# Optimization experiments

Hardware: AMD Instinct MI355X
Metric: run time of the kernel (lower is better)

## Reference

```python
import jax, jax.numpy as jnp
import numpy as np
from jax.scipy.linalg import cho_solve

B, IN, H, Y, K = 16384, 128, 512, 32, 8
EPS = 1e-6


def setup_inputs() -> dict:
    key = jax.random.key(0)
    ks = jax.random.split(key, 7)
    s_in = 1.0 / np.sqrt(IN)
    s_h = 1.0 / np.sqrt(H)
    x = jax.random.normal(ks[0], (B, IN), dtype=jnp.float32)
    W1 = jax.random.normal(ks[1], (IN, H), dtype=jnp.float32) * s_in
    b1 = jnp.zeros((H,), dtype=jnp.float32)
    WD = jax.random.normal(ks[2], (H, Y), dtype=jnp.float32) * s_h
    bD = jnp.zeros((Y,), dtype=jnp.float32)
    WV = jax.random.normal(ks[3], (H, Y * K), dtype=jnp.float32) * s_h
    bV = jnp.zeros((Y * K,), dtype=jnp.float32)
    return {"x": x, "W1": W1, "b1": b1, "WD": WD, "bD": bD, "WV": WV, "bV": bV}


def reference(x, W1, b1, WD, bD, WV, bV):
    # backbone: simple MLP feature extractor
    feat = jax.nn.relu(x @ W1 + b1)                      # [B, H]
    # head (low_rank mode): D > 0 diagonal scales, V low-rank factor
    D = jax.nn.softplus(feat @ WD + bD) + 1e-3           # [B, Y]
    V = (feat @ WV + bV).reshape(-1, Y, K)               # [B, Y, K]

    inv_D2 = 1.0 / (D * D)                               # [B, Y]
    W = V * inv_D2[..., None]                            # A_inv @ V, [B, Y, K]
    # M = I_K + V^T A_inv V  (Woodbury capacitance), [B, K, K]
    M = jnp.eye(K, dtype=V.dtype) + jnp.einsum("byk,byj->bkj", V, W)
    L_M = jnp.linalg.cholesky(M)
    eyeK = jnp.broadcast_to(jnp.eye(K, dtype=V.dtype), M.shape)
    M_inv = cho_solve((L_M, True), eyeK)                 # torch.cholesky_inverse
    # Sigma_inv = A_inv - W M_inv W^T, [B, Y, Y]
    correction = jnp.einsum("byk,bkj,bzj->byz", W, M_inv, W)
    A_inv = inv_D2[:, :, None] * jnp.eye(Y, dtype=V.dtype)
    Sigma_inv = A_inv - correction

    eigvals, eigvecs = jnp.linalg.eigh(Sigma_inv)        # [B,Y], [B,Y,Y]
    sqrt_vals = jnp.sqrt(eigvals + EPS)
    # Sigma_inv_sqrt = Q diag(sqrt(lam)) Q^T
    Sigma_inv_sqrt = jnp.einsum("byk,bk,bzk->byz", eigvecs, sqrt_vals, eigvecs)
    return Sigma_inv_sqrt
```

## Files before the change

kernel.cpp:

```cpp
#include <hip/hip_runtime.h>
#include <math.h>


template <int ACT>
__global__ __launch_bounds__(256) void gemm_act(const float* __restrict__ A,
                                                const float* __restrict__ Bm,
                                                const float* __restrict__ bias,
                                                float* __restrict__ C,
                                                int M, int N, int K) {
  __shared__ float As[16][68];
  __shared__ float Bs[16][68];
  const int tid = threadIdx.x;
  const int bm = blockIdx.y * 64;
  const int bn = blockIdx.x * 64;
  const int tx = tid & 15, ty = tid >> 4;
  const int arow = tid >> 2, acol4 = (tid & 3) << 2;
  const int brow = tid >> 4, bcol4 = (tid & 15) << 2;
  float acc[4][4] = {};

  for (int k0 = 0; k0 < K; k0 += 16) {
    float4 av = *(const float4*)(A + (size_t)(bm + arow) * K + (k0 + acol4));
    As[acol4 + 0][arow] = av.x;
    As[acol4 + 1][arow] = av.y;
    As[acol4 + 2][arow] = av.z;
    As[acol4 + 3][arow] = av.w;
    float4 bv = make_float4(0.f, 0.f, 0.f, 0.f);
    if (bn + bcol4 < N)
      bv = *(const float4*)(Bm + (size_t)(k0 + brow) * N + (bn + bcol4));
    *(float4*)&Bs[brow][bcol4] = bv;
    __syncthreads();
#pragma unroll
    for (int k = 0; k < 16; ++k) {
      float ar[4], br[4];
#pragma unroll
      for (int i = 0; i < 4; ++i) ar[i] = As[k][(ty << 2) + i];
#pragma unroll
      for (int j = 0; j < 4; ++j) br[j] = Bs[k][(tx << 2) + j];
#pragma unroll
      for (int i = 0; i < 4; ++i)
#pragma unroll
        for (int j = 0; j < 4; ++j) acc[i][j] = fmaf(ar[i], br[j], acc[i][j]);
    }
    __syncthreads();
  }

#pragma unroll
  for (int i = 0; i < 4; ++i) {
    int row = bm + (ty << 2) + i;
#pragma unroll
    for (int j = 0; j < 4; ++j) {
      int col = bn + (tx << 2) + j;
      if (col < N) {
        float v = acc[i][j] + bias[col];
        if (ACT == 1) v = fmaxf(v, 0.f);
        if (ACT == 2) {
          float sp = fmaxf(v, 0.f) + log1pf(expf(-fabsf(v)));
          float D = sp + 1e-3f;
          v = 1.f / (D * D);
        }
        C[(size_t)row * N + col] = v;
      }
    }
  }
}

__global__ __launch_bounds__(64) void woodbury_sqrtm_os(
    const float* __restrict__ invD2g, const float* __restrict__ Vg,
    float* __restrict__ out) {
  const int lane = threadIdx.x;
  const int h = lane >> 5;
  const int j = lane & 31;
  const int b = blockIdx.x * 2 + h;

  __shared__ __align__(16) char lds[9216];
  float* Vb = (float*)lds;
  float* ad = (float*)(lds + 2048);
  double* Md = (double*)(lds + 2304);
  double* Ud = (double*)(lds + 3456);
  float* FT = (float*)lds;

  const float a_d = invD2g[(size_t)b * 32 + j];
  const float4 v0 = *(const float4*)(Vg + (size_t)b * 256 + j * 8);
  const float4 v1 = *(const float4*)(Vg + (size_t)b * 256 + j * 8 + 4);
  {
    float* vb = Vb + (h * 32 + j) * 8;
    *(float4*)vb = v0;
    *(float4*)(vb + 4) = v1;
    ad[h * 32 + j] = a_d;
  }
  __syncthreads();

  {
    const int e0 = 2 * j;
    const int i0 = e0 >> 3, c0 = e0 & 7;
    double m0 = (i0 == c0) ? 1.0 : 0.0;
    double m1 = (i0 == c0 + 1) ? 1.0 : 0.0;
    const float* vbase = Vb + h * 256;
    const float* abase = ad + h * 32;
    for (int y = 0; y < 32; ++y) {
      double dv = (double)abase[y];
      double vi = (double)vbase[y * 8 + i0] * dv;
      m0 += vi * (double)vbase[y * 8 + c0];
      m1 += vi * (double)vbase[y * 8 + c0 + 1];
    }
    Md[h * 72 + i0 * 9 + c0] = m0;
    Md[h * 72 + i0 * 9 + c0 + 1] = m1;
  }
  __syncthreads();

  if (j == 0) {
    double* M = Md + h * 72;
    for (int k = 0; k < 8; ++k) {
      double d = M[k * 9 + k];
      for (int i2 = 0; i2 < k; ++i2) {
        double l = M[k * 9 + i2];
        d -= l * l;
      }
      double lkk = sqrt(fmax(d, 1e-30));
      M[k * 9 + k] = lkk;
      double inv = 1.0 / lkk;
      for (int r = k + 1; r < 8; ++r) {
        double vv = M[r * 9 + k];
        for (int i2 = 0; i2 < k; ++i2) vv -= M[r * 9 + i2] * M[k * 9 + i2];
        M[r * 9 + k] = vv * inv;
      }
    }
  }
  __syncthreads();

  double u[8];
  {
    const double* L = Md + h * 72;
    float w[8] = {v0.x * a_d, v0.y * a_d, v0.z * a_d, v0.w * a_d,
                  v1.x * a_d, v1.y * a_d, v1.z * a_d, v1.w * a_d};
#pragma unroll
    for (int jj = 0; jj < 8; ++jj) {
      double vv = (double)w[jj];
      for (int i2 = 0; i2 < jj; ++i2) vv -= u[i2] * L[jj * 9 + i2];
      u[jj] = vv / L[jj * 9 + jj];
    }
    double* ur = Ud + (h * 32 + j) * 9;
#pragma unroll
    for (int k = 0; k < 8; ++k) ur[k] = u[k];
  }
  __syncthreads();

  float g[32];
#pragma unroll
  for (int i = 0; i < 32; ++i) {
    const double* ui = Ud + (h * 32 + i) * 9;
    double acc = 0.0;
#pragma unroll
    for (int k = 0; k < 8; ++k) acc += ui[k] * u[k];
    double val = -acc;
    if (i == j) val += (double)a_d + 1e-6;
    g[i] = (float)val;
  }
  __syncthreads();

  float bnorm = 0.f;
  for (int sweep = 0; sweep < 8; ++sweep) {
    bnorm = 0.f;
#pragma unroll
    for (int k = 0; k < 32; ++k) bnorm = fmaf(g[k], g[k], bnorm);
    for (int m = 1; m < 32; ++m) {
      const int partner = lane ^ m;
      const bool isp = j < (j ^ m);
      float pb = __shfl(bnorm, partner, 64);
      float pg[32];
#pragma unroll
      for (int k = 0; k < 32; ++k) pg[k] = __shfl(g[k], partner, 64);
      float apq = 0.f;
#pragma unroll
      for (int k = 0; k < 32; ++k) apq = fmaf(g[k], pg[k], apq);
      const float app = isp ? bnorm : pb;
      const float aqq = isp ? pb : bnorm;
      const bool big = fabsf(apq) > 1e-30f;
      const float sapq = big ? apq : 1.f;
      const float tau = (aqq - app) / (2.f * sapq);
      float t = copysignf(1.f, tau) / (fabsf(tau) + sqrtf(fmaf(tau, tau, 1.f)));
      t = big ? t : 0.f;
      const float c = 1.f / sqrtf(fmaf(t, t, 1.f));
      const float s = t * c;
      const float se = isp ? -s : s;
#pragma unroll
      for (int k = 0; k < 32; ++k) g[k] = fmaf(se, pg[k], c * g[k]);
      bnorm = fmaxf(isp ? fmaf(-t, apq, bnorm) : fmaf(t, apq, bnorm), 0.f);
    }
  }

  float b2 = 0.f;
#pragma unroll
  for (int k = 0; k < 32; ++k) b2 = fmaf(g[k], g[k], b2);
  b2 = fmaxf(b2, 1e-20f);
  const float lam = sqrtf(b2);
  const float sw = 1.f / sqrtf(lam * sqrtf(lam));

  float* FTh = FT + h * 1152;
#pragma unroll
  for (int i = 0; i < 32; ++i) FTh[i * 36 + j] = g[i] * sw;
  __syncthreads();

  float rj[32];
  {
    const float4* rowj = (const float4*)(FTh + j * 36);
#pragma unroll
    for (int c4 = 0; c4 < 8; ++c4) {
      float4 v = rowj[c4];
      rj[4 * c4 + 0] = v.x;
      rj[4 * c4 + 1] = v.y;
      rj[4 * c4 + 2] = v.z;
      rj[4 * c4 + 3] = v.w;
    }
  }
  float* ob = out + (size_t)b * 1024;
  for (int i = 0; i < 32; ++i) {
    const float4* rowi = (const float4*)(FTh + i * 36);
    float acc = 0.f;
#pragma unroll
    for (int c4 = 0; c4 < 8; ++c4) {
      float4 v = rowi[c4];
      acc = fmaf(v.x, rj[4 * c4 + 0], acc);
      acc = fmaf(v.y, rj[4 * c4 + 1], acc);
      acc = fmaf(v.z, rj[4 * c4 + 2], acc);
      acc = fmaf(v.w, rj[4 * c4 + 3], acc);
    }
    ob[i * 32 + j] = acc;
  }
}

extern "C" void kernel_launch(void* const* d_in, const int* in_sizes, int n_in,
                              void* d_out, int out_size, void* d_ws,
                              size_t ws_size, hipStream_t stream) {
  const float* x = (const float*)d_in[0];
  const float* W1 = (const float*)d_in[1];
  const float* b1 = (const float*)d_in[2];
  const float* WD = (const float*)d_in[3];
  const float* bD = (const float*)d_in[4];
  const float* WV = (const float*)d_in[5];
  const float* bV = (const float*)d_in[6];
  float* out = (float*)d_out;

  float* feat = out;
  float* invD2 = (float*)d_ws;
  float* V = (float*)d_ws + (size_t)16384 * 32;

  gemm_act<1><<<dim3(512 / 64, 16384 / 64), 256, 0, stream>>>(
      x, W1, b1, feat, 16384, 512, 128);
  gemm_act<2><<<dim3(1, 16384 / 64), 256, 0, stream>>>(
      feat, WD, bD, invD2, 16384, 32, 512);
  gemm_act<0><<<dim3(256 / 64, 16384 / 64), 256, 0, stream>>>(
      feat, WV, bV, V, 16384, 256, 512);
  woodbury_sqrtm_os<<<16384 / 2, 64, 0, stream>>>(invD2, V, out);
}
```

Measured before the change: 1.004 ms.

## Vectorize one-sided Jacobi with packed float2 math, bpermute shuffles, fewer sweeps

Rewrites the one-sided Jacobi eigen-sweep inner loop to hold columns as float2 vectors so the compiler can emit packed FMA instructions. Shuffles now use ds_bpermute directly, and dot-product reductions are split across four accumulators to shorten dependency chains. The sweep count drops from 8 to 7, and launch bounds now request 2 blocks per CU. Cutting a sweep trades convergence accuracy for less work and could raise output error for poorly conditioned matrices.

```diff
diff --git a/kernel.cpp b/kernel.cpp
--- a/kernel.cpp
+++ b/kernel.cpp
@@ -1,6 +1,8 @@
 #include <hip/hip_runtime.h>
 #include <math.h>
 
+
+typedef float v2f __attribute__((ext_vector_type(2)));
 
 template <int ACT>
 __global__ __launch_bounds__(256) void gemm_act(const float* __restrict__ A,
@@ -64,7 +66,7 @@
   }
 }
 
-__global__ __launch_bounds__(64) void woodbury_sqrtm_os(
+__global__ __launch_bounds__(64, 2) void woodbury_sqrtm_os(
     const float* __restrict__ invD2g, const float* __restrict__ Vg,
     float* __restrict__ out) {
   const int lane = threadIdx.x;
@@ -145,7 +147,7 @@
   }
   __syncthreads();
 
-  float g[32];
+  v2f g2[16];
 #pragma unroll
   for (int i = 0; i < 32; ++i) {
     const double* ui = Ud + (h * 32 + i) * 9;
@@ -154,25 +156,51 @@
     for (int k = 0; k < 8; ++k) acc += ui[k] * u[k];
     double val = -acc;
     if (i == j) val += (double)a_d + 1e-6;
-    g[i] = (float)val;
-  }
-  __syncthreads();
-
+    if (i & 1)
+      g2[i >> 1].y = (float)val;
+    else
+      g2[i >> 1].x = (float)val;
+  }
+  __syncthreads();
+
+  const int lane4 = lane << 2;
   float bnorm = 0.f;
-  for (int sweep = 0; sweep < 8; ++sweep) {
-    bnorm = 0.f;
-#pragma unroll
-    for (int k = 0; k < 32; ++k) bnorm = fmaf(g[k], g[k], bnorm);
+  for (int sweep = 0; sweep < 7; ++sweep) {
+    {
+      v2f a0 = {0.f, 0.f}, a1 = {0.f, 0.f}, a2 = {0.f, 0.f}, a3 = {0.f, 0.f};
+#pragma unroll
+      for (int k = 0; k < 16; k += 4) {
+        a0 += g2[k + 0] * g2[k + 0];
+        a1 += g2[k + 1] * g2[k + 1];
+        a2 += g2[k + 2] * g2[k + 2];
+        a3 += g2[k + 3] * g2[k + 3];
+      }
+      v2f t01 = a0 + a1, t23 = a2 + a3, tt = t01 + t23;
+      bnorm = tt.x + tt.y;
+    }
     for (int m = 1; m < 32; ++m) {
-      const int partner = lane ^ m;
+      const int pb4 = lane4 ^ (m << 2);
       const bool isp = j < (j ^ m);
-      float pb = __shfl(bnorm, partner, 64);
-      float pg[32];
-#pragma unroll
-      for (int k = 0; k < 32; ++k) pg[k] = __shfl(g[k], partner, 64);
-      float apq = 0.f;
-#pragma unroll
-      for (int k = 0; k < 32; ++k) apq = fmaf(g[k], pg[k], apq);
+      v2f pg2[16];
+#pragma unroll
+      for (int k = 0; k < 16; ++k) {
+        pg2[k].x = __int_as_float(
+            __builtin_amdgcn_ds_bpermute(pb4, __float_as_int(g2[k].x)));
+        pg2[k].y = __int_as_float(
+            __builtin_amdgcn_ds_bpermute(pb4, __float_as_int(g2[k].y)));
+      }
+      const float pb = __int_as_float(
+          __builtin_amdgcn_ds_bpermute(pb4, __float_as_int(bnorm)));
+      v2f d0 = {0.f, 0.f}, d1 = {0.f, 0.f}, d2 = {0.f, 0.f}, d3 = {0.f, 0.f};
+#pragma unroll
+      for (int k = 0; k < 16; k += 4) {
+        d0 += g2[k + 0] * pg2[k + 0];
+        d1 += g2[k + 1] * pg2[k + 1];
+        d2 += g2[k + 2] * pg2[k + 2];
+        d3 += g2[k + 3] * pg2[k + 3];
+      }
+      v2f s01 = d0 + d1, s23 = d2 + d3, st = s01 + s23;
+      const float apq = st.x + st.y;
       const float app = isp ? bnorm : pb;
       const float aqq = isp ? pb : bnorm;
       const bool big = fabsf(apq) > 1e-30f;
@@ -183,22 +211,36 @@
       const float c = 1.f / sqrtf(fmaf(t, t, 1.f));
       const float s = t * c;
       const float se = isp ? -s : s;
-#pragma unroll
-      for (int k = 0; k < 32; ++k) g[k] = fmaf(se, pg[k], c * g[k]);
-      bnorm = fmaxf(isp ? fmaf(-t, apq, bnorm) : fmaf(t, apq, bnorm), 0.f);
-    }
-  }
-
-  float b2 = 0.f;
-#pragma unroll
-  for (int k = 0; k < 32; ++k) b2 = fmaf(g[k], g[k], b2);
-  b2 = fmaxf(b2, 1e-20f);
+      const v2f cc = {c, c};
+      const v2f sse = {se, se};
+#pragma unroll
+      for (int k = 0; k < 16; ++k) g2[k] = cc * g2[k] + sse * pg2[k];
+      bnorm = fmaxf(fmaf(isp ? -t : t, apq, bnorm), 0.f);
+    }
+  }
+
+  float b2;
+  {
+    v2f a0 = {0.f, 0.f}, a1 = {0.f, 0.f}, a2 = {0.f, 0.f}, a3 = {0.f, 0.f};
+#pragma unroll
+    for (int k = 0; k < 16; k += 4) {
+      a0 += g2[k + 0] * g2[k + 0];
+      a1 += g2[k + 1] * g2[k + 1];
+      a2 += g2[k + 2] * g2[k + 2];
+      a3 += g2[k + 3] * g2[k + 3];
+    }
+    v2f t01 = a0 + a1, t23 = a2 + a3, tt = t01 + t23;
+    b2 = fmaxf(tt.x + tt.y, 1e-20f);
+  }
   const float lam = sqrtf(b2);
   const float sw = 1.f / sqrtf(lam * sqrtf(lam));
 
   float* FTh = FT + h * 1152;
 #pragma unroll
-  for (int i = 0; i < 32; ++i) FTh[i * 36 + j] = g[i] * sw;
+  for (int i = 0; i < 16; ++i) {
+    FTh[(2 * i + 0) * 36 + j] = g2[i].x * sw;
+    FTh[(2 * i + 1) * 36 + j] = g2[i].y * sw;
+  }
   __syncthreads();
 
   float rj[32];
```

After: 885.3 us. 1.13x faster.

## Restructure one-sided Jacobi eigensolver to two columns per lane, four matrices per wave

Applied to the files above, without the earlier changes.

The Woodbury/Jacobi kernel now assigns two columns per lane, so one 64-lane wave handles four 32x32 matrices instead of two. Each lane rotates its own pair locally, then exchanges with a partner through ds_bpermute. Only 15 partner rounds per sweep are needed, and sweeps drop from 8 to 7. It also uses packed float2 FMAs, fast rcp/rsq intrinsics and float storage for the triangular-solve output, which cuts shuffle traffic and arithmetic but doubles register pressure per lane. The reduced sweep count and lower-precision intrinsics may slightly change convergence accuracy.

```diff
diff --git a/kernel.cpp b/kernel.cpp
--- a/kernel.cpp
+++ b/kernel.cpp
@@ -1,6 +1,8 @@
 #include <hip/hip_runtime.h>
 #include <math.h>
 
+
+typedef float v2f __attribute__((ext_vector_type(2)));
 
 template <int ACT>
 __global__ __launch_bounds__(256) void gemm_act(const float* __restrict__ A,
@@ -64,168 +66,255 @@
   }
 }
 
-__global__ __launch_bounds__(64) void woodbury_sqrtm_os(
+#define PIN2(x) asm("" : "+v"(x))
+
+__device__ __forceinline__ float bperm1(int addr, float v) {
+  return __int_as_float(__builtin_amdgcn_ds_bpermute(addr, __float_as_int(v)));
+}
+
+__device__ __forceinline__ float dotcols(const v2f* a, const v2f* b) {
+  v2f d0 = {0.f, 0.f}, d1 = {0.f, 0.f}, d2 = {0.f, 0.f}, d3 = {0.f, 0.f};
+#pragma unroll
+  for (int k = 0; k < 16; k += 4) {
+    d0 += a[k + 0] * b[k + 0];
+    d1 += a[k + 1] * b[k + 1];
+    d2 += a[k + 2] * b[k + 2];
+    d3 += a[k + 3] * b[k + 3];
+  }
+  v2f s01 = d0 + d1, s23 = d2 + d3, st = s01 + s23;
+  return st.x + st.y;
+}
+
+__device__ __forceinline__ void crossrot(v2f* O, float& nO, v2f* P, float& nP,
+                                         bool isp) {
+  const float apq = dotcols(O, P);
+  const float app = isp ? nO : nP;
+  const float aqq = isp ? nP : nO;
+  const bool big = fabsf(apq) > 1e-30f;
+  const float sapq = big ? apq : 1.f;
+  const float tau = (aqq - app) * 0.5f * __builtin_amdgcn_rcpf(sapq);
+  float t = copysignf(
+      __builtin_amdgcn_rcpf(fabsf(tau) + sqrtf(fmaf(tau, tau, 1.f))), tau);
+  t = big ? t : 0.f;
+  const float c = __builtin_amdgcn_rsqf(fmaf(t, t, 1.f));
+  const float s = t * c;
+  const float se = isp ? -s : s;
+  const v2f cc = {c, c};
+  const v2f vse = {se, se};
+#pragma unroll
+  for (int k = 0; k < 16; ++k) {
+    v2f o = O[k];
+    O[k] = cc * o + vse * P[k];
+    P[k] = cc * P[k] - vse * o;
+  }
+  const float d = t * apq;
+  nO = fmaxf(isp ? nO - d : nO + d, 0.f);
+  nP = fmaxf(isp ? nP + d : nP - d, 0.f);
+}
+
+__global__ __launch_bounds__(64, 2) void woodbury_sqrtm_blk(
     const float* __restrict__ invD2g, const float* __restrict__ Vg,
     float* __restrict__ out) {
   const int lane = threadIdx.x;
-  const int h = lane >> 5;
-  const int j = lane & 31;
-  const int b = blockIdx.x * 2 + h;
-
-  __shared__ __align__(16) char lds[9216];
-  float* Vb = (float*)lds;
-  float* ad = (float*)(lds + 2048);
-  double* Md = (double*)(lds + 2304);
-  double* Ud = (double*)(lds + 3456);
+  const int q = lane >> 4;
+  const int l = lane & 15;
+  const int b = blockIdx.x * 4 + q;
+  const int ca = 2 * l;
+
+  __shared__ __align__(16) char lds[17408];
+  float* adS = (float*)lds;
+  float* Vs = (float*)(lds + 512);
+  double* Md = (double*)(lds + 4608);
+  float* Uf = (float*)(lds + 6912);
   float* FT = (float*)lds;
 
-  const float a_d = invD2g[(size_t)b * 32 + j];
-  const float4 v0 = *(const float4*)(Vg + (size_t)b * 256 + j * 8);
-  const float4 v1 = *(const float4*)(Vg + (size_t)b * 256 + j * 8 + 4);
+  const float2 adp = *(const float2*)(invD2g + (size_t)b * 32 + ca);
+  const float ada = adp.x, adb = adp.y;
+  adS[q * 32 + ca] = ada;
+  adS[q * 32 + ca + 1] = adb;
+  const float4 va0 = *(const float4*)(Vg + (size_t)b * 256 + ca * 8);
+  const float4 va1 = *(const float4*)(Vg + (size_t)b * 256 + ca * 8 + 4);
+  const float4 vb0 = *(const float4*)(Vg + (size_t)b * 256 + ca * 8 + 8);
+  const float4 vb1 = *(const float4*)(Vg + (size_t)b * 256 + ca * 8 + 12);
+  *(float4*)(Vs + (q * 32 + ca) * 8) = va0;
+  *(float4*)(Vs + (q * 32 + ca) * 8 + 4) = va1;
+  *(float4*)(Vs + (q * 32 + ca + 1) * 8) = vb0;
+  *(float4*)(Vs + (q * 32 + ca + 1) * 8 + 4) = vb1;
+  __syncthreads();
+
   {
-    float* vb = Vb + (h * 32 + j) * 8;
-    *(float4*)vb = v0;
-    *(float4*)(vb + 4) = v1;
-    ad[h * 32 + j] = a_d;
-  }
-  __syncthreads();
-
-  {
-    const int e0 = 2 * j;
-    const int i0 = e0 >> 3, c0 = e0 & 7;
-    double m0 = (i0 == c0) ? 1.0 : 0.0;
-    double m1 = (i0 == c0 + 1) ? 1.0 : 0.0;
-    const float* vbase = Vb + h * 256;
-    const float* abase = ad + h * 32;
+    const int r = l >> 1, c0 = (l & 1) * 4;
+    double m0 = 0, m1 = 0, m2 = 0, m3 = 0;
+    const float* vq = Vs + q * 256;
+    const float* aq = adS + q * 32;
     for (int y = 0; y < 32; ++y) {
-      double dv = (double)abase[y];
-      double vi = (double)vbase[y * 8 + i0] * dv;
-      m0 += vi * (double)vbase[y * 8 + c0];
-      m1 += vi * (double)vbase[y * 8 + c0 + 1];
-    }
-    Md[h * 72 + i0 * 9 + c0] = m0;
-    Md[h * 72 + i0 * 9 + c0 + 1] = m1;
-  }
-  __syncthreads();
-
-  if (j == 0) {
-    double* M = Md + h * 72;
+      const double pr = (double)vq[y * 8 + r] * (double)aq[y];
+      m0 += pr * (double)vq[y * 8 + c0 + 0];
+      m1 += pr * (double)vq[y * 8 + c0 + 1];
+      m2 += pr * (double)vq[y * 8 + c0 + 2];
+      m3 += pr * (double)vq[y * 8 + c0 + 3];
+    }
+    double* Mq = Md + q * 72;
+    Mq[r * 9 + c0 + 0] = m0 + ((r == c0 + 0) ? 1.0 : 0.0);
+    Mq[r * 9 + c0 + 1] = m1 + ((r == c0 + 1) ? 1.0 : 0.0);
+    Mq[r * 9 + c0 + 2] = m2 + ((r == c0 + 2) ? 1.0 : 0.0);
+    Mq[r * 9 + c0 + 3] = m3 + ((r == c0 + 3) ? 1.0 : 0.0);
+  }
+  __syncthreads();
+
+  if (l == 0) {
+    double* M = Md + q * 72;
     for (int k = 0; k < 8; ++k) {
       double d = M[k * 9 + k];
-      for (int i2 = 0; i2 < k; ++i2) {
-        double l = M[k * 9 + i2];
-        d -= l * l;
-      }
-      double lkk = sqrt(fmax(d, 1e-30));
+      for (int i = 0; i < k; ++i) {
+        const double lv = M[k * 9 + i];
+        d -= lv * lv;
+      }
+      const double lkk = sqrt(fmax(d, 1e-30));
       M[k * 9 + k] = lkk;
-      double inv = 1.0 / lkk;
+      const double inv = 1.0 / lkk;
       for (int r = k + 1; r < 8; ++r) {
-        double vv = M[r * 9 + k];
-        for (int i2 = 0; i2 < k; ++i2) vv -= M[r * 9 + i2] * M[k * 9 + i2];
-        M[r * 9 + k] = vv * inv;
-      }
-    }
-  }
-  __syncthreads();
-
-  double u[8];
+        double v = M[r * 9 + k];
+        for (int i = 0; i < k; ++i) v -= M[r * 9 + i] * M[k * 9 + i];
+        M[r * 9 + k] = v * inv;
+      }
+    }
+  }
+  __syncthreads();
+
+  float ua[8], ub[8];
   {
-    const double* L = Md + h * 72;
-    float w[8] = {v0.x * a_d, v0.y * a_d, v0.z * a_d, v0.w * a_d,
-                  v1.x * a_d, v1.y * a_d, v1.z * a_d, v1.w * a_d};
+    const double* L = Md + q * 72;
+    const float wa[8] = {va0.x * ada, va0.y * ada, va0.z * ada, va0.w * ada,
+                         va1.x * ada, va1.y * ada, va1.z * ada, va1.w * ada};
+    const float wb[8] = {vb0.x * adb, vb0.y * adb, vb0.z * adb, vb0.w * adb,
+                         vb1.x * adb, vb1.y * adb, vb1.z * adb, vb1.w * adb};
+    double ta[8], tb[8];
 #pragma unroll
     for (int jj = 0; jj < 8; ++jj) {
-      double vv = (double)w[jj];
-      for (int i2 = 0; i2 < jj; ++i2) vv -= u[i2] * L[jj * 9 + i2];
-      u[jj] = vv / L[jj * 9 + jj];
-    }
-    double* ur = Ud + (h * 32 + j) * 9;
-#pragma unroll
-    for (int k = 0; k < 8; ++k) ur[k] = u[k];
-  }
-  __syncthreads();
-
-  float g[32];
-#pragma unroll
-  for (int i = 0; i < 32; ++i) {
-    const double* ui = Ud + (h * 32 + i) * 9;
-    double acc = 0.0;
-#pragma unroll
-    for (int k = 0; k < 8; ++k) acc += ui[k] * u[k];
-    double val = -acc;
-    if (i == j) val += (double)a_d + 1e-6;
-    g[i] = (float)val;
-  }
-  __syncthreads();
-
-  float bnorm = 0.f;
-  for (int sweep = 0; sweep < 8; ++sweep) {
-    bnorm = 0.f;
-#pragma unroll
-    for (int k = 0; k < 32; ++k) bnorm = fmaf(g[k], g[k], bnorm);
-    for (int m = 1; m < 32; ++m) {
-      const int partner = lane ^ m;
-      const bool isp = j < (j ^ m);
-      float pb = __shfl(bnorm, partner, 64);
-      float pg[32];
-#pragma unroll
-      for (int k = 0; k < 32; ++k) pg[k] = __shfl(g[k], partner, 64);
-      float apq = 0.f;
-#pragma unroll
-      for (int k = 0; k < 32; ++k) apq = fmaf(g[k], pg[k], apq);
-      const float app = isp ? bnorm : pb;
-      const float aqq = isp ? pb : bnorm;
-      const bool big = fabsf(apq) > 1e-30f;
-      const float sapq = big ? apq : 1.f;
-      const float tau = (aqq - app) / (2.f * sapq);
-      float t = copysignf(1.f, tau) / (fabsf(tau) + sqrtf(fmaf(tau, tau, 1.f)));
-      t = big ? t : 0.f;
-      const float c = 1.f / sqrtf(fmaf(t, t, 1.f));
-      const float s = t * c;
-      const float se = isp ? -s : s;
-#pragma unroll
-      for (int k = 0; k < 32; ++k) g[k] = fmaf(se, pg[k], c * g[k]);
-      bnorm = fmaxf(isp ? fmaf(-t, apq, bnorm) : fmaf(t, apq, bnorm), 0.f);
-    }
-  }
-
-  float b2 = 0.f;
-#pragma unroll
-  for (int k = 0; k < 32; ++k) b2 = fmaf(g[k], g[k], b2);
-  b2 = fmaxf(b2, 1e-20f);
-  const float lam = sqrtf(b2);
-  const float sw = 1.f / sqrtf(lam * sqrtf(lam));
-
-  float* FTh = FT + h * 1152;
-#pragma unroll
-  for (int i = 0; i < 32; ++i) FTh[i * 36 + j] = g[i] * sw;
-  __syncthreads();
-
-  float rj[32];
+      double sa = (double)wa[jj], sb = (double)wb[jj];
+      for (int i = 0; i < jj; ++i) {
+        const double lv = L[jj * 9 + i];
+        sa -= ta[i] * lv;
+        sb -= tb[i] * lv;
+      }
+      const double inv = 1.0 / L[jj * 9 + jj];
+      ta[jj] = sa * inv;
+      tb[jj] = sb * inv;
+      ua[jj] = (float)ta[jj];
+      ub[jj] = (float)tb[jj];
+    }
+    float* ur = Uf + q * 256;
+#pragma unroll
+    for (int k = 0; k < 8; ++k) {
+      ur[ca * 8 + k] = ua[k];
+      ur[(ca + 1) * 8 + k] = ub[k];
+    }
+  }
+  __syncthreads();
+
+  v2f gA[16], gB[16];
   {
-    const float4* rowj = (const float4*)(FTh + j * 36);
+    const float* uq = Uf + q * 256;
+    for (int i = 0; i < 32; ++i) {
+      const float* ui = uq + i * 8;
+      float sa = 0.f, sb = 0.f;
+#pragma unroll
+      for (int k = 0; k < 8; ++k) {
+        sa = fmaf(ui[k], ua[k], sa);
+        sb = fmaf(ui[k], ub[k], sb);
+      }
+      float gva = -sa, gvb = -sb;
+      if (i == ca) gva += ada + 1e-6f;
+      if (i == ca + 1) gvb += adb + 1e-6f;
+      if (i & 1) {
+        gA[i >> 1].y = gva;
+        gB[i >> 1].y = gvb;
+      } else {
+        gA[i >> 1].x = gva;
+        gB[i >> 1].x = gvb;
+      }
+    }
+  }
+  __syncthreads();
+
+  const int self4 = lane << 2;
+  float nA = 0.f, nB = 0.f;
+  for (int sweep = 0; sweep < 7; ++sweep) {
+    nA = dotcols(gA, gA);
+    nB = dotcols(gB, gB);
+    for (int m = 1; m < 16; ++m) {
+      crossrot(gA, nA, gB, nB, true);
+      const int pa4 = self4 ^ (m << 2);
+      v2f pA[16], pB[16];
+#pragma unroll
+      for (int k = 0; k < 16; ++k) {
+        v2f t0, t1;
+        t0.x = bperm1(pa4, gA[k].x);
+        t0.y = bperm1(pa4, gA[k].y);
+        PIN2(t0);
+        pA[k] = t0;
+        t1.x = bperm1(pa4, gB[k].x);
+        t1.y = bperm1(pa4, gB[k].y);
+        PIN2(t1);
+        pB[k] = t1;
+      }
+      float pnA = bperm1(pa4, nA);
+      float pnB = bperm1(pa4, nB);
+      const bool isp = l < (l ^ m);
+      crossrot(gA, nA, pA, pnA, isp);
+      crossrot(gB, nB, pB, pnB, isp);
+      crossrot(gA, nA, pB, pnB, isp);
+      crossrot(gB, nB, pA, pnA, isp);
+    }
+  }
+
+  float b2a = fmaxf(dotcols(gA, gA), 1e-20f);
+  float b2b = fmaxf(dotcols(gB, gB), 1e-20f);
+  const float la = sqrtf(b2a), lb = sqrtf(b2b);
+  const float swa = 1.f / sqrtf(la * sqrtf(la));
+  const float swb = 1.f / sqrtf(lb * sqrtf(lb));
+
+  float* FTq = FT + q * 1088;
+#pragma unroll
+  for (int k = 0; k < 16; ++k) {
+    float2 w0 = {gA[k].x * swa, gB[k].x * swb};
+    float2 w1 = {gA[k].y * swa, gB[k].y * swb};
+    *(float2*)(FTq + (2 * k) * 34 + ca) = w0;
+    *(float2*)(FTq + (2 * k + 1) * 34 + ca) = w1;
+  }
+  __syncthreads();
+
+  float ra[32], rb[32];
+  {
+    const float4* rowa = (const float4*)(FTq + ca * 34);
+    const float4* rowb = (const float4*)(FTq + (ca + 1) * 34);
 #pragma unroll
     for (int c4 = 0; c4 < 8; ++c4) {
-      float4 v = rowj[c4];
-      rj[4 * c4 + 0] = v.x;
-      rj[4 * c4 + 1] = v.y;
-      rj[4 * c4 + 2] = v.z;
-      rj[4 * c4 + 3] = v.w;
+      const float4 x = rowa[c4], y = rowb[c4];
+      ra[4 * c4 + 0] = x.x; ra[4 * c4 + 1] = x.y;
+      ra[4 * c4 + 2] = x.z; ra[4 * c4 + 3] = x.w;
+      rb[4 * c4 + 0] = y.x; rb[4 * c4 + 1] = y.y;
+      rb[4 * c4 + 2] = y.z; rb[4 * c4 + 3] = y.w;
     }
   }
   float* ob = out + (size_t)b * 1024;
   for (int i = 0; i < 32; ++i) {
-    const float4* rowi = (const float4*)(FTh + i * 36);
-    float acc = 0.f;
+    const float4* ri = (const float4*)(FTq + i * 34);
+    float sa = 0.f, sb = 0.f;
 #pragma unroll
     for (int c4 = 0; c4 < 8; ++c4) {
-      float4 v = rowi[c4];
-      acc = fmaf(v.x, rj[4 * c4 + 0], acc);
-      acc = fmaf(v.y, rj[4 * c4 + 1], acc);
-      acc = fmaf(v.z, rj[4 * c4 + 2], acc);
-      acc = fmaf(v.w, rj[4 * c4 + 3], acc);
-    }
-    ob[i * 32 + j] = acc;
+      const float4 v = ri[c4];
+      sa = fmaf(v.x, ra[4 * c4 + 0], sa);
+      sa = fmaf(v.y, ra[4 * c4 + 1], sa);
+      sa = fmaf(v.z, ra[4 * c4 + 2], sa);
+      sa = fmaf(v.w, ra[4 * c4 + 3], sa);
+      sb = fmaf(v.x, rb[4 * c4 + 0], sb);
+      sb = fmaf(v.y, rb[4 * c4 + 1], sb);
+      sb = fmaf(v.z, rb[4 * c4 + 2], sb);
+      sb = fmaf(v.w, rb[4 * c4 + 3], sb);
+    }
+    *(float2*)(ob + i * 32 + ca) = make_float2(sa, sb);
   }
 }
 
@@ -251,5 +340,5 @@
       feat, WD, bD, invD2, 16384, 32, 512);
   gemm_act<0><<<dim3(256 / 64, 16384 / 64), 256, 0, stream>>>(
       feat, WV, bV, V, 16384, 256, 512);
-  woodbury_sqrtm_os<<<16384 / 2, 64, 0, stream>>>(invD2, V, out);
-}
+  woodbury_sqrtm_blk<<<16384 / 4, 64, 0, stream>>>(invD2, V, out);
+}
```

Measured after the change: 808.7 us. 1.24x faster.
